# Kernel optimization log

Measured on AMD Instinct MI355X. Metric: run time of the kernel, lower is better.

## Reference

```python
import jax, jax.numpy as jnp
import numpy as np

N_EMBED = 2048
N_HEAD = 16
HEAD_DIM = N_EMBED // N_HEAD
ROPE_BASE = 500000


def _rope_cos_sin(T, dim, base):
    # torchtune RotaryPositionalEmbeddings: interleaved pairs
    inv_freq = 1.0 / (base ** (jnp.arange(0, dim, 2, dtype=jnp.float32) / dim))  # [dim/2]
    pos = jnp.arange(T, dtype=jnp.float32)
    ang = pos[:, None] * inv_freq[None, :]  # [T, dim/2]
    return jnp.cos(ang), jnp.sin(ang)


def _apply_rope(x, cos, sin):
    # x: [B, T, H, D]; cos/sin: [T, D/2] -> broadcast [1, T, 1, D/2]
    c = cos[None, :, None, :]
    s = sin[None, :, None, :]
    x1 = x[..., 0::2]
    x2 = x[..., 1::2]
    r1 = x1 * c - x2 * s
    r2 = x2 * c + x1 * s
    return jnp.stack([r1, r2], axis=-1).reshape(x.shape)


def setup_inputs() -> dict:
    key = jax.random.key(0)
    k1, k2, k3 = jax.random.split(key, 3)
    B, T, C = 4, 2048, N_EMBED
    x = jax.random.normal(k1, (B, T, C), dtype=jnp.float32)
    Wqkv = jax.random.normal(k2, (C, 3 * C), dtype=jnp.float32) * 0.02
    Wproj = jax.random.normal(k3, (C, C), dtype=jnp.float32) * 0.02
    return {"x": x, "Wqkv": Wqkv, "Wproj": Wproj}


def reference(x, Wqkv, Wproj):
    B, T, C = x.shape
    H, D = N_HEAD, HEAD_DIM
    qkv = x @ Wqkv  # [B, T, 3C]
    q, k, v = jnp.split(qkv, 3, axis=2)
    q = q.reshape(B, T, H, D)
    k = k.reshape(B, T, H, D)
    v = v.reshape(B, T, H, D)
    cos, sin = _rope_cos_sin(T, D, ROPE_BASE)
    q = _apply_rope(q, cos, sin)
    k = _apply_rope(k, cos, sin)
    scale = 1.0 / jnp.sqrt(jnp.float32(D))
    # causal SDPA: scores [B, H, T, T]
    scores = jnp.einsum('bqhd,bkhd->bhqk', q, k) * scale
    mask = jnp.tril(jnp.ones((T, T), dtype=bool))
    scores = jnp.where(mask[None, None, :, :], scores, jnp.float32(-1e30))
    attn = jax.nn.softmax(scores, axis=-1)
    y = jnp.einsum('bhqk,bkhd->bqhd', attn, v).reshape(B, T, C)
    return y @ Wproj
```

## Files before the change

kernel.cpp:

```cpp
#include <hip/hip_runtime.h>
#include <math.h>

#define NB 4
#define TT 2048
#define CC 2048
#define HH 16
#define DD 128
#define N3 6144
#define MM 8192
#define BH 64

typedef short bf8 __attribute__((ext_vector_type(8)));
typedef float f32x4 __attribute__((ext_vector_type(4)));
typedef unsigned short u16x8 __attribute__((ext_vector_type(8)));
typedef unsigned short u16;

constexpr float SCALE_QK  = 0.08838834764831843f;
constexpr float NEG_ALPHA = -0.20503692777194262f;

__device__ __forceinline__ u16 f2bf(float x) {
    unsigned int u = __float_as_uint(x);
    u += 0x7fffu + ((u >> 16) & 1u);
    return (u16)(u >> 16);
}
__device__ __forceinline__ float bf2f(u16 h) { return __uint_as_float(((unsigned int)h) << 16); }

__device__ __forceinline__ void gl_lds16(const u16* g, u16* l) {
    __builtin_amdgcn_global_load_lds(reinterpret_cast<const unsigned int*>(g),
                                     reinterpret_cast<unsigned int*>(l), 16, 0, 0);
}
__device__ __forceinline__ f32x4 MFMA(bf8 a, bf8 b, f32x4 c) {
    return __builtin_amdgcn_mfma_f32_16x16x32_bf16(a, b, c, 0, 0, 0);
}

#define BAR()    __builtin_amdgcn_s_barrier()
#define SCHED0() __builtin_amdgcn_sched_barrier(0)
#define WAIT_LGKM0() do { asm volatile("s_waitcnt lgkmcnt(0)" ::: "memory"); SCHED0(); } while (0)
#define WAIT_VM4()   do { asm volatile("s_waitcnt vmcnt(4)"   ::: "memory"); SCHED0(); } while (0)
#define WAIT_VM0()   do { asm volatile("s_waitcnt vmcnt(0)"   ::: "memory"); SCHED0(); } while (0)

__global__ void rope_tab_k(float* __restrict__ tab) {
    int t = blockIdx.x, p = threadIdx.x;
    float inv = expf((float)p * NEG_ALPHA);
    float s, c;
    sincosf((float)t * inv, &s, &c);
    tab[(t * 64 + p) * 2]     = c;
    tab[(t * 64 + p) * 2 + 1] = s;
}

__global__ __launch_bounds__(256) void split_x_k(const float* __restrict__ X,
                                                 u16* __restrict__ H, u16* __restrict__ L) {
    size_t base = ((size_t)blockIdx.x * 256 + threadIdx.x) * 16;
    #pragma unroll
    for (int g = 0; g < 2; ++g) {
        u16x8 hv, lv;
        #pragma unroll
        for (int j = 0; j < 8; j += 4) {
            float4 a = *(const float4*)(X + base + g * 8 + j);
            float xs[4] = {a.x, a.y, a.z, a.w};
            #pragma unroll
            for (int q = 0; q < 4; ++q) {
                u16 h = f2bf(xs[q]);
                hv[j + q] = h;
                lv[j + q] = f2bf(xs[q] - bf2f(h));
            }
        }
        *(u16x8*)&H[base + g * 8] = hv;
        *(u16x8*)&L[base + g * 8] = lv;
    }
}

__global__ __launch_bounds__(256) void splitT_k(const float* __restrict__ W,
                                                u16* __restrict__ OH, u16* __restrict__ OL,
                                                int Kd, int Nd) {
    __shared__ float tile[64][68];
    int k0 = blockIdx.x * 64, n0 = blockIdx.y * 64;
    {
        int r = threadIdx.x >> 2, cg = threadIdx.x & 3;
        const float* src = W + (size_t)(k0 + r) * Nd + n0 + cg * 16;
        #pragma unroll
        for (int j = 0; j < 4; ++j)
            *(float4*)&tile[r][cg * 16 + j * 4] = *(const float4*)(src + j * 4);
    }
    __syncthreads();
    int nl = threadIdx.x >> 2, kg = threadIdx.x & 3;
    u16x8 hv[2], lv[2];
    #pragma unroll
    for (int j = 0; j < 16; ++j) {
        float v = tile[kg * 16 + j][nl];
        u16 h = f2bf(v);
        hv[j >> 3][j & 7] = h;
        lv[j >> 3][j & 7] = f2bf(v - bf2f(h));
    }
    size_t off = (size_t)(n0 + nl) * Kd + k0 + kg * 16;
    *(u16x8*)&OH[off]     = hv[0];
    *(u16x8*)&OH[off + 8] = hv[1];
    *(u16x8*)&OL[off]     = lv[0];
    *(u16x8*)&OL[off + 8] = lv[1];
}

template<int MODE>
__global__ __launch_bounds__(512, 2) void gemm8p(
    const u16* __restrict__ Ahp, const u16* __restrict__ Alp,
    const u16* __restrict__ Bhp, const u16* __restrict__ Blp,
    u16* __restrict__ Qh, u16* __restrict__ Ql,
    u16* __restrict__ Kbo, u16* __restrict__ Vto,
    const float* __restrict__ tab, float* __restrict__ Out)
{
    __shared__ u16 SM[66048];

    const int tid = threadIdx.x;
    const int w = tid >> 6, ln = tid & 63;
    const int lo4 = ln & 15, hi4 = ln >> 4;
    const int wr = w >> 2, wc = w & 3;
    const int m0 = blockIdx.x * 256, n0 = blockIdx.y * 256;
    const int NKT = 96;

    f32x4 acc[8][4];
    #pragma unroll
    for (int i = 0; i < 8; ++i)
        #pragma unroll
        for (int j = 0; j < 4; ++j) acc[i][j] = (f32x4){0.f, 0.f, 0.f, 0.f};

    auto stage = [&](int s) {
        if (s >= 4 * NKT) return;
        const int tau = s >> 2, j = s & 3;
        const int c2 = tau & 1, op = j >> 1, hf = j & 1;
        const int tdiv = tau >> 5, tmod = tau & 31;
        const u16* plane;
        int row0;
        if (op == 0) { plane = (tdiv == 1) ? Alp : Ahp; row0 = m0 + hf * 128; }
        else         { plane = (tdiv == 2) ? Blp : Bhp; row0 = n0 + hf * 128; }
        u16* dst = SM + (op ? 32768 : 0) + (c2 * 2 + hf) * 8192;
        #pragma unroll
        for (int i = 0; i < 2; ++i) {
            int L = i * 8192 + tid * 16;
            int r = L >> 7;
            int c = (L >> 4) & 7;
            int cs = c ^ (r & 7);
            gl_lds16(plane + (size_t)(row0 + r) * 2048 + tmod * 64 + cs * 8,
                     dst + (L >> 1));
        }
    };

    #pragma unroll
    for (int s = 0; s < 6; ++s) stage(s);
    WAIT_VM4();
    BAR();

    bf8 a03[4][2], a47[4][2], b01[2][2], b23[2][2];
    const int brow0 = (wc & 1) * 64;

    for (int t = 0; t < NKT; ++t) {
        const int c2 = t & 1;
        const u16* Ab = SM + (c2 * 2 + wr) * 8192;
        const u16* Bb = SM + 32768 + (c2 * 2 + (wc >> 1)) * 8192;

        #pragma unroll
        for (int mf = 0; mf < 4; ++mf) {
            int rr = mf * 16 + lo4, s7 = rr & 7;
            a03[mf][0] = *(const bf8*)&Ab[rr * 64 + ((hi4 ^ s7)) * 8];
            a03[mf][1] = *(const bf8*)&Ab[rr * 64 + (((4 + hi4) ^ s7)) * 8];
        }
        #pragma unroll
        for (int nf = 0; nf < 2; ++nf) {
            int rr = brow0 + nf * 16 + lo4, s7 = rr & 7;
            b01[nf][0] = *(const bf8*)&Bb[rr * 64 + ((hi4 ^ s7)) * 8];
            b01[nf][1] = *(const bf8*)&Bb[rr * 64 + (((4 + hi4) ^ s7)) * 8];
        }
        stage(4 * t + 6);
        BAR(); WAIT_LGKM0();
        __builtin_amdgcn_s_setprio(1);
        #pragma unroll
        for (int mf = 0; mf < 4; ++mf)
            #pragma unroll
            for (int nf = 0; nf < 2; ++nf) {
                acc[mf][nf] = MFMA(a03[mf][0], b01[nf][0], acc[mf][nf]);
                acc[mf][nf] = MFMA(a03[mf][1], b01[nf][1], acc[mf][nf]);
            }
        __builtin_amdgcn_s_setprio(0);
        BAR();

        #pragma unroll
        for (int mf = 0; mf < 4; ++mf) {
            int rr = 64 + mf * 16 + lo4, s7 = rr & 7;
            a47[mf][0] = *(const bf8*)&Ab[rr * 64 + ((hi4 ^ s7)) * 8];
            a47[mf][1] = *(const bf8*)&Ab[rr * 64 + (((4 + hi4) ^ s7)) * 8];
        }
        stage(4 * t + 7);
        BAR(); WAIT_LGKM0();
        __builtin_amdgcn_s_setprio(1);
        #pragma unroll
        for (int mf = 0; mf < 4; ++mf)
            #pragma unroll
            for (int nf = 0; nf < 2; ++nf) {
                acc[4 + mf][nf] = MFMA(a47[mf][0], b01[nf][0], acc[4 + mf][nf]);
                acc[4 + mf][nf] = MFMA(a47[mf][1], b01[nf][1], acc[4 + mf][nf]);
            }
        __builtin_amdgcn_s_setprio(0);
        BAR();

        #pragma unroll
        for (int nf = 0; nf < 2; ++nf) {
            int rr = brow0 + 32 + nf * 16 + lo4, s7 = rr & 7;
            b23[nf][0] = *(const bf8*)&Bb[rr * 64 + ((hi4 ^ s7)) * 8];
            b23[nf][1] = *(const bf8*)&Bb[rr * 64 + (((4 + hi4) ^ s7)) * 8];
        }
        stage(4 * t + 8);
        BAR(); WAIT_LGKM0();
        __builtin_amdgcn_s_setprio(1);
        #pragma unroll
        for (int mf = 0; mf < 4; ++mf)
            #pragma unroll
            for (int nf = 0; nf < 2; ++nf) {
                acc[mf][2 + nf] = MFMA(a03[mf][0], b23[nf][0], acc[mf][2 + nf]);
                acc[mf][2 + nf] = MFMA(a03[mf][1], b23[nf][1], acc[mf][2 + nf]);
            }
        __builtin_amdgcn_s_setprio(0);
        BAR();

        stage(4 * t + 9);
        BAR();
        __builtin_amdgcn_s_setprio(1);
        #pragma unroll
        for (int mf = 0; mf < 4; ++mf)
            #pragma unroll
            for (int nf = 0; nf < 2; ++nf) {
                acc[4 + mf][2 + nf] = MFMA(a47[mf][0], b23[nf][0], acc[4 + mf][2 + nf]);
                acc[4 + mf][2 + nf] = MFMA(a47[mf][1], b23[nf][1], acc[4 + mf][2 + nf]);
            }
        __builtin_amdgcn_s_setprio(0);
        if (t < NKT - 2)       { WAIT_VM4(); }
        else if (t == NKT - 2) { WAIT_VM0(); }
        BAR();
    }

    if (MODE == 1) {
        #pragma unroll
        for (int mf = 0; mf < 8; ++mf)
            #pragma unroll
            for (int r = 0; r < 4; ++r) {
                int m = m0 + wr * 128 + mf * 16 + hi4 * 4 + r;
                float* rowp = Out + (size_t)m * CC + n0 + wc * 64;
                #pragma unroll
                for (int nf = 0; nf < 4; ++nf)
                    rowp[nf * 16 + lo4] = acc[mf][nf][r];
            }
        return;
    }

    const int sec = n0 >> 11;
    const int hh0 = (n0 >> 7) & 15;
    if (sec < 2) {
        #pragma unroll
        for (int mf = 0; mf < 8; ++mf)
            #pragma unroll
            for (int r = 0; r < 4; ++r) {
                int m = m0 + wr * 128 + mf * 16 + hi4 * 4 + r;
                int t = m & 2047, b = m >> 11;
                #pragma unroll
                for (int nf = 0; nf < 4; ++nf) {
                    int nl = wc * 64 + nf * 16 + lo4;
                    int h = hh0 + (nl >> 7), d = nl & 127;
                    float v = acc[mf][nf][r];
                    float o = __shfl_xor(v, 1);
                    const float2 cs2 = *(const float2*)&tab[(((size_t)t << 6) + (d >> 1)) * 2];
                    float rv = (ln & 1) ? (v * cs2.x + o * cs2.y)
                                        : (v * cs2.x - o * cs2.y);
                    size_t off = (((size_t)(b * HH + h)) * TT + t) * DD + d;
                    if (sec == 0) {
                        rv *= SCALE_QK;
                        u16 hv = f2bf(rv);
                        Qh[off] = hv;
                        Ql[off] = f2bf(rv - bf2f(hv));
                    } else {
                        Kbo[off] = f2bf(rv);
                    }
                }
            }
    } else {
        BAR();
        #pragma unroll
        for (int mf = 0; mf < 8; ++mf)
            #pragma unroll
            for (int r = 0; r < 4; ++r) {
                int tl = wr * 128 + mf * 16 + hi4 * 4 + r;
                #pragma unroll
                for (int nf = 0; nf < 4; ++nf) {
                    int nl = wc * 64 + nf * 16 + lo4;
                    SM[tl * 258 + nl] = f2bf(acc[mf][nf][r]);
                }
            }
        BAR();
        int nl = tid >> 1, th = tid & 1;
        int head = hh0 + (nl >> 7), d = nl & 127;
        int b = m0 >> 11, t0 = m0 & 2047;
        size_t base = (((size_t)(b * HH + head)) * DD + d) * TT + t0 + th * 128;
        #pragma unroll
        for (int g = 0; g < 16; ++g) {
            u16x8 vv;
            #pragma unroll
            for (int j = 0; j < 8; ++j) vv[j] = SM[(th * 128 + g * 8 + j) * 258 + nl];
            *(u16x8*)&Vto[base + g * 8] = vv;
        }
    }
}

__global__ __launch_bounds__(256) void attn_mfma(
    const u16* __restrict__ Qhp, const u16* __restrict__ Qlp,
    const u16* __restrict__ Kb,  const u16* __restrict__ Vt,
    u16* __restrict__ Yh, u16* __restrict__ Yl)
{
    __shared__ u16 Ks[64 * 128];
    __shared__ u16 Vs[128 * 64];
    __shared__ u16 Ps[4][16 * 64];

    const int tid = threadIdx.x;
    const int w = tid >> 6, ln = tid & 63;
    const int lo4 = ln & 15, hi4 = ln >> 4;
    const int qt = blockIdx.x, bh = blockIdx.y;
    const int q0 = qt * 64;

    const size_t qoff = ((size_t)bh * TT + q0) * DD;
    #pragma unroll
    for (int i = 0; i < 4; ++i) {
        int L = i * 4096 + tid * 16;
        int r = L >> 8;
        int c = (L >> 4) & 15;
        int cs = c ^ (r & 7);
        gl_lds16(Qhp + qoff + r * DD + cs * 8, &Ks[L >> 1]);
        gl_lds16(Qlp + qoff + r * DD + cs * 8, &Vs[L >> 1]);
    }
    __syncthreads();
    bf8 qh[4], ql[4];
    {
        int r = w * 16 + lo4;
        #pragma unroll
        for (int ks = 0; ks < 4; ++ks) {
            int ch = (ks * 4 + hi4) ^ (r & 7);
            qh[ks] = *(const bf8*)&Ks[r * 128 + ch * 8];
            ql[ks] = *(const bf8*)&Vs[r * 128 + ch * 8];
        }
    }

    f32x4 O[8];
    #pragma unroll
    for (int i = 0; i < 8; ++i) O[i] = (f32x4){0.f, 0.f, 0.f, 0.f};
    float m_r[4] = {-1e30f, -1e30f, -1e30f, -1e30f};
    float l_r[4] = {0.f, 0.f, 0.f, 0.f};

    for (int kt = 0; kt <= qt; ++kt) {
        __syncthreads();
        const size_t koff = ((size_t)bh * TT + kt * 64) * DD;
        #pragma unroll
        for (int i = 0; i < 4; ++i) {
            int L = i * 4096 + tid * 16;
            int r = L >> 8;
            int c = (L >> 4) & 15;
            int cs = c ^ (r & 7);
            gl_lds16(Kb + koff + r * DD + cs * 8, &Ks[L >> 1]);
        }
        #pragma unroll
        for (int i = 0; i < 4; ++i) {
            int L = i * 4096 + tid * 16;
            int r = L >> 7;
            int c = (L >> 4) & 7;
            int cs = c ^ (r & 7);
            gl_lds16(Vt + ((size_t)bh * DD + r) * TT + kt * 64 + cs * 8, &Vs[L >> 1]);
        }
        __syncthreads();

        f32x4 sf[4];
        #pragma unroll
        for (int nf = 0; nf < 4; ++nf) {
            f32x4 a2 = (f32x4){0.f, 0.f, 0.f, 0.f};
            int kr = nf * 16 + lo4;
            #pragma unroll
            for (int ks = 0; ks < 4; ++ks) {
                int ch = (ks * 4 + hi4) ^ (kr & 7);
                bf8 bb = *(const bf8*)&Ks[kr * 128 + ch * 8];
                a2 = MFMA(qh[ks], bb, a2);
                a2 = MFMA(ql[ks], bb, a2);
            }
            sf[nf] = a2;
        }
        if (kt == qt) {
            #pragma unroll
            for (int nf = 0; nf < 4; ++nf)
                #pragma unroll
                for (int r = 0; r < 4; ++r) {
                    int kg = kt * 64 + nf * 16 + lo4;
                    int qg = q0 + w * 16 + hi4 * 4 + r;
                    if (kg > qg) sf[nf][r] = -1e30f;
                }
        }
        #pragma unroll
        for (int r = 0; r < 4; ++r) {
            float mx = fmaxf(fmaxf(sf[0][r], sf[1][r]), fmaxf(sf[2][r], sf[3][r]));
            mx = fmaxf(mx, __shfl_xor(mx, 1));
            mx = fmaxf(mx, __shfl_xor(mx, 2));
            mx = fmaxf(mx, __shfl_xor(mx, 4));
            mx = fmaxf(mx, __shfl_xor(mx, 8));
            float mn = fmaxf(m_r[r], mx);
            float al = __expf(m_r[r] - mn);
            m_r[r] = mn;
            float rs = 0.f;
            #pragma unroll
            for (int nf = 0; nf < 4; ++nf) {
                float p = __expf(sf[nf][r] - mn);
                sf[nf][r] = p;
                rs += p;
            }
            rs += __shfl_xor(rs, 1);
            rs += __shfl_xor(rs, 2);
            rs += __shfl_xor(rs, 4);
            rs += __shfl_xor(rs, 8);
            l_r[r] = l_r[r] * al + rs;
            #pragma unroll
            for (int nf2 = 0; nf2 < 8; ++nf2) O[nf2][r] *= al;
        }
        u16* pw = &Ps[w][0];
        #pragma unroll
        for (int r = 0; r < 4; ++r) {
            int row = hi4 * 4 + r;
            int sw = (row & 7) << 3;
            #pragma unroll
            for (int nf = 0; nf < 4; ++nf)
                pw[row * 64 + ((nf * 16 + lo4) ^ sw)] = f2bf(sf[nf][r]);
        }
        bf8 pa[2];
        {
            int row = lo4, s3 = row & 7;
            pa[0] = *(const bf8*)&pw[row * 64 + ((hi4 ^ s3) * 8)];
            pa[1] = *(const bf8*)&pw[row * 64 + (((4 + hi4) ^ s3) * 8)];
        }
        #pragma unroll
        for (int nf2 = 0; nf2 < 8; ++nf2) {
            int vr = nf2 * 16 + lo4;
            #pragma unroll
            for (int ks = 0; ks < 2; ++ks) {
                int ch = (ks * 4 + hi4) ^ (vr & 7);
                bf8 vb = *(const bf8*)&Vs[vr * 64 + ch * 8];
                O[nf2] = MFMA(pa[ks], vb, O[nf2]);
            }
        }
    }

    const int b = bh >> 4, h = bh & 15;
    #pragma unroll
    for (int r = 0; r < 4; ++r) {
        float inv = 1.0f / l_r[r];
        int t = q0 + w * 16 + hi4 * 4 + r;
        size_t rowo = ((size_t)(b * TT + t)) * CC + h * DD;
        #pragma unroll
        for (int nf2 = 0; nf2 < 8; ++nf2) {
            float val = O[nf2][r] * inv;
            u16 hv = f2bf(val);
            Yh[rowo + nf2 * 16 + lo4] = hv;
            Yl[rowo + nf2 * 16 + lo4] = f2bf(val - bf2f(hv));
        }
    }
}

extern "C" void kernel_launch(void* const* d_in, const int* in_sizes, int n_in,
                              void* d_out, int out_size, void* d_ws, size_t ws_size,
                              hipStream_t stream)
{
    const float* X     = (const float*)d_in[0];
    const float* Wqkv  = (const float*)d_in[1];
    const float* Wproj = (const float*)d_in[2];

    char* W = (char*)d_ws;
    float* tab = (float*)W;
    u16* Wqh = (u16*)(W + (1u << 20));
    u16* Wql = Wqh + 12582912;
    u16* Wph = Wql + 12582912;
    u16* Wpl = Wph + 4194304;
    u16* Xh  = Wpl + 4194304;
    u16* Xl  = Xh + 16777216;
    u16* Kb  = Xl + 16777216;
    u16* Vt  = Kb + 16777216;

    u16* Qh = (u16*)d_out;
    u16* Ql = Qh + 16777216;

    u16* Yh = Xh;
    u16* Yl = Xl;

    rope_tab_k<<<dim3(2048), 64, 0, stream>>>(tab);
    split_x_k<<<dim3(4096), 256, 0, stream>>>(X, Xh, Xl);
    splitT_k<<<dim3(32, 96), 256, 0, stream>>>(Wqkv, Wqh, Wql, 2048, 6144);
    splitT_k<<<dim3(32, 32), 256, 0, stream>>>(Wproj, Wph, Wpl, 2048, 2048);

    gemm8p<0><<<dim3(32, 24), 512, 0, stream>>>(Xh, Xl, Wqh, Wql,
                                                Qh, Ql, Kb, Vt, tab, nullptr);
    attn_mfma<<<dim3(32, 64), 256, 0, stream>>>(Qh, Ql, Kb, Vt, Yh, Yl);
    gemm8p<1><<<dim3(32, 8), 512, 0, stream>>>(Yh, Yl, Wph, Wpl,
                                               nullptr, nullptr, nullptr, nullptr,
                                               nullptr, (float*)d_out);
}
```

Baseline: 1.231 ms.

## Drop weight low-part GEMM pass and rewrite attention with 128-row double-buffered tiles

The weights are now split into a bf16 high part only, so both GEMMs run two bf16 passes (Ah*Bh, Al*Bh) instead of three, cutting K-iterations from 96 to 64 and the weight-split work. The attention kernel now gives each block 128 query rows, double-buffers K/V tiles with async global-to-LDS loads, and pairs light and heavy causal tiles in the block ordering. It also skips the O rescale when no row maximum grows. Losing the weight low part reduces accuracy, and the larger attention tile adds register pressure.

```diff
diff --git a/kernel.cpp b/kernel.cpp
--- a/kernel.cpp
+++ b/kernel.cpp
@@ -36,6 +36,7 @@
 #define BAR()    __builtin_amdgcn_s_barrier()
 #define SCHED0() __builtin_amdgcn_sched_barrier(0)
 #define WAIT_LGKM0() do { asm volatile("s_waitcnt lgkmcnt(0)" ::: "memory"); SCHED0(); } while (0)
+#define WAIT_VM8()   do { asm volatile("s_waitcnt vmcnt(8)"   ::: "memory"); SCHED0(); } while (0)
 #define WAIT_VM4()   do { asm volatile("s_waitcnt vmcnt(4)"   ::: "memory"); SCHED0(); } while (0)
 #define WAIT_VM0()   do { asm volatile("s_waitcnt vmcnt(0)"   ::: "memory"); SCHED0(); } while (0)
 
@@ -70,8 +71,8 @@
     }
 }
 
-__global__ __launch_bounds__(256) void splitT_k(const float* __restrict__ W,
-                                                u16* __restrict__ OH, u16* __restrict__ OL,
+__global__ __launch_bounds__(256) void splitT_h(const float* __restrict__ W,
+                                                u16* __restrict__ OH,
                                                 int Kd, int Nd) {
     __shared__ float tile[64][68];
     int k0 = blockIdx.x * 64, n0 = blockIdx.y * 64;
@@ -84,25 +85,19 @@
     }
     __syncthreads();
     int nl = threadIdx.x >> 2, kg = threadIdx.x & 3;
-    u16x8 hv[2], lv[2];
-    #pragma unroll
-    for (int j = 0; j < 16; ++j) {
-        float v = tile[kg * 16 + j][nl];
-        u16 h = f2bf(v);
-        hv[j >> 3][j & 7] = h;
-        lv[j >> 3][j & 7] = f2bf(v - bf2f(h));
-    }
+    u16x8 hv[2];
+    #pragma unroll
+    for (int j = 0; j < 16; ++j)
+        hv[j >> 3][j & 7] = f2bf(tile[kg * 16 + j][nl]);
     size_t off = (size_t)(n0 + nl) * Kd + k0 + kg * 16;
     *(u16x8*)&OH[off]     = hv[0];
     *(u16x8*)&OH[off + 8] = hv[1];
-    *(u16x8*)&OL[off]     = lv[0];
-    *(u16x8*)&OL[off + 8] = lv[1];
 }
 
 template<int MODE>
 __global__ __launch_bounds__(512, 2) void gemm8p(
     const u16* __restrict__ Ahp, const u16* __restrict__ Alp,
-    const u16* __restrict__ Bhp, const u16* __restrict__ Blp,
+    const u16* __restrict__ Bhp,
     u16* __restrict__ Qh, u16* __restrict__ Ql,
     u16* __restrict__ Kbo, u16* __restrict__ Vto,
     const float* __restrict__ tab, float* __restrict__ Out)
@@ -114,7 +109,7 @@
     const int lo4 = ln & 15, hi4 = ln >> 4;
     const int wr = w >> 2, wc = w & 3;
     const int m0 = blockIdx.x * 256, n0 = blockIdx.y * 256;
-    const int NKT = 96;
+    const int NKT = 64;
 
     f32x4 acc[8][4];
     #pragma unroll
@@ -129,8 +124,8 @@
         const int tdiv = tau >> 5, tmod = tau & 31;
         const u16* plane;
         int row0;
-        if (op == 0) { plane = (tdiv == 1) ? Alp : Ahp; row0 = m0 + hf * 128; }
-        else         { plane = (tdiv == 2) ? Blp : Bhp; row0 = n0 + hf * 128; }
+        if (op == 0) { plane = tdiv ? Alp : Ahp; row0 = m0 + hf * 128; }
+        else         { plane = Bhp;              row0 = n0 + hf * 128; }
         u16* dst = SM + (op ? 32768 : 0) + (c2 * 2 + hf) * 8192;
         #pragma unroll
         for (int i = 0; i < 2; ++i) {
@@ -306,160 +301,207 @@
     }
 }
 
-__global__ __launch_bounds__(256) void attn_mfma(
+__global__ __launch_bounds__(256, 2) void attn128(
     const u16* __restrict__ Qhp, const u16* __restrict__ Qlp,
     const u16* __restrict__ Kb,  const u16* __restrict__ Vt,
     u16* __restrict__ Yh, u16* __restrict__ Yl)
 {
-    __shared__ u16 Ks[64 * 128];
-    __shared__ u16 Vs[128 * 64];
-    __shared__ u16 Ps[4][16 * 64];
+    __shared__ u16 SM[40960];
 
     const int tid = threadIdx.x;
     const int w = tid >> 6, ln = tid & 63;
     const int lo4 = ln & 15, hi4 = ln >> 4;
-    const int qt = blockIdx.x, bh = blockIdx.y;
-    const int q0 = qt * 64;
+    const int bx = blockIdx.x;
+    const int qt = (bx & 1) ? (15 - (bx >> 1)) : (bx >> 1);
+    const int bh = blockIdx.y;
+    const int q0 = qt * 128;
+    const int last = 2 * qt + 1;
 
     const size_t qoff = ((size_t)bh * TT + q0) * DD;
     #pragma unroll
-    for (int i = 0; i < 4; ++i) {
+    for (int i = 0; i < 8; ++i) {
         int L = i * 4096 + tid * 16;
-        int r = L >> 8;
-        int c = (L >> 4) & 15;
+        int r = L >> 8, c = (L >> 4) & 15;
         int cs = c ^ (r & 7);
-        gl_lds16(Qhp + qoff + r * DD + cs * 8, &Ks[L >> 1]);
-        gl_lds16(Qlp + qoff + r * DD + cs * 8, &Vs[L >> 1]);
-    }
-    __syncthreads();
-    bf8 qh[4], ql[4];
-    {
-        int r = w * 16 + lo4;
+        gl_lds16(Qhp + qoff + r * DD + cs * 8, &SM[L >> 1]);
+        gl_lds16(Qlp + qoff + r * DD + cs * 8, &SM[16384 + (L >> 1)]);
+    }
+    WAIT_VM0();
+    BAR();
+    bf8 qh[2][4], ql[2][4];
+    #pragma unroll
+    for (int mf = 0; mf < 2; ++mf) {
+        int rq = w * 32 + mf * 16 + lo4, s7 = rq & 7;
         #pragma unroll
         for (int ks = 0; ks < 4; ++ks) {
-            int ch = (ks * 4 + hi4) ^ (r & 7);
-            qh[ks] = *(const bf8*)&Ks[r * 128 + ch * 8];
-            ql[ks] = *(const bf8*)&Vs[r * 128 + ch * 8];
-        }
-    }
-
-    f32x4 O[8];
-    #pragma unroll
-    for (int i = 0; i < 8; ++i) O[i] = (f32x4){0.f, 0.f, 0.f, 0.f};
-    float m_r[4] = {-1e30f, -1e30f, -1e30f, -1e30f};
-    float l_r[4] = {0.f, 0.f, 0.f, 0.f};
-
-    for (int kt = 0; kt <= qt; ++kt) {
-        __syncthreads();
-        const size_t koff = ((size_t)bh * TT + kt * 64) * DD;
+            int ch = (ks * 4 + hi4) ^ s7;
+            qh[mf][ks] = *(const bf8*)&SM[rq * 128 + ch * 8];
+            ql[mf][ks] = *(const bf8*)&SM[16384 + rq * 128 + ch * 8];
+        }
+    }
+    WAIT_LGKM0();
+    BAR();
+
+    auto stageKV = [&](int kt2, int buf) {
+        const size_t koff = ((size_t)bh * TT + kt2 * 64) * DD;
+        u16* kd = &SM[buf * 8192];
         #pragma unroll
         for (int i = 0; i < 4; ++i) {
             int L = i * 4096 + tid * 16;
-            int r = L >> 8;
-            int c = (L >> 4) & 15;
-            int cs = c ^ (r & 7);
-            gl_lds16(Kb + koff + r * DD + cs * 8, &Ks[L >> 1]);
-        }
+            int r = L >> 8, c = (L >> 4) & 15, cs = c ^ (r & 7);
+            gl_lds16(Kb + koff + r * DD + cs * 8, kd + (L >> 1));
+        }
+        const size_t voff = (size_t)bh * DD * TT + (size_t)kt2 * 64;
+        u16* vd = &SM[16384 + buf * 8192];
         #pragma unroll
         for (int i = 0; i < 4; ++i) {
             int L = i * 4096 + tid * 16;
-            int r = L >> 7;
-            int c = (L >> 4) & 7;
-            int cs = c ^ (r & 7);
-            gl_lds16(Vt + ((size_t)bh * DD + r) * TT + kt * 64 + cs * 8, &Vs[L >> 1]);
-        }
-        __syncthreads();
-
-        f32x4 sf[4];
+            int r = L >> 7, c = (L >> 4) & 7, cs = c ^ (r & 7);
+            gl_lds16(Vt + voff + (size_t)r * TT + cs * 8, vd + (L >> 1));
+        }
+    };
+    stageKV(0, 0);
+
+    f32x4 O[2][8];
+    #pragma unroll
+    for (int mf = 0; mf < 2; ++mf)
+        #pragma unroll
+        for (int i = 0; i < 8; ++i) O[mf][i] = (f32x4){0.f, 0.f, 0.f, 0.f};
+    float m_r[2][4], l_r[2][4];
+    #pragma unroll
+    for (int mf = 0; mf < 2; ++mf)
+        #pragma unroll
+        for (int r = 0; r < 4; ++r) { m_r[mf][r] = -1e30f; l_r[mf][r] = 0.f; }
+
+    for (int kt = 0; kt <= last; ++kt) {
+        const int cur = kt & 1;
+        if (kt < last) { stageKV(kt + 1, cur ^ 1); WAIT_VM8(); }
+        else           { WAIT_VM0(); }
+        BAR();
+        const u16* Kcur = &SM[cur * 8192];
+        const u16* Vcur = &SM[16384 + cur * 8192];
+
+        f32x4 sf[2][4];
         #pragma unroll
         for (int nf = 0; nf < 4; ++nf) {
-            f32x4 a2 = (f32x4){0.f, 0.f, 0.f, 0.f};
-            int kr = nf * 16 + lo4;
+            f32x4 s0 = (f32x4){0.f, 0.f, 0.f, 0.f};
+            f32x4 s1 = (f32x4){0.f, 0.f, 0.f, 0.f};
+            int kr = nf * 16 + lo4, s7 = kr & 7;
             #pragma unroll
             for (int ks = 0; ks < 4; ++ks) {
-                int ch = (ks * 4 + hi4) ^ (kr & 7);
-                bf8 bb = *(const bf8*)&Ks[kr * 128 + ch * 8];
-                a2 = MFMA(qh[ks], bb, a2);
-                a2 = MFMA(ql[ks], bb, a2);
-            }
-            sf[nf] = a2;
-        }
-        if (kt == qt) {
-            #pragma unroll
-            for (int nf = 0; nf < 4; ++nf)
+                bf8 bb = *(const bf8*)&Kcur[kr * 128 + ((ks * 4 + hi4) ^ s7) * 8];
+                s0 = MFMA(qh[0][ks], bb, s0);
+                s0 = MFMA(ql[0][ks], bb, s0);
+                s1 = MFMA(qh[1][ks], bb, s1);
+                s1 = MFMA(ql[1][ks], bb, s1);
+            }
+            sf[0][nf] = s0; sf[1][nf] = s1;
+        }
+        if (kt >= 2 * qt) {
+            #pragma unroll
+            for (int mf = 0; mf < 2; ++mf)
+                #pragma unroll
+                for (int nf = 0; nf < 4; ++nf)
+                    #pragma unroll
+                    for (int r = 0; r < 4; ++r) {
+                        int kg = kt * 64 + nf * 16 + lo4;
+                        int qg = q0 + w * 32 + mf * 16 + hi4 * 4 + r;
+                        if (kg > qg) sf[mf][nf][r] = -1e30f;
+                    }
+        }
+
+        #pragma unroll
+        for (int mf = 0; mf < 2; ++mf) {
+            float mx[4];
+            #pragma unroll
+            for (int r = 0; r < 4; ++r) {
+                float m2 = fmaxf(fmaxf(sf[mf][0][r], sf[mf][1][r]),
+                                 fmaxf(sf[mf][2][r], sf[mf][3][r]));
+                m2 = fmaxf(m2, __shfl_xor(m2, 1));
+                m2 = fmaxf(m2, __shfl_xor(m2, 2));
+                m2 = fmaxf(m2, __shfl_xor(m2, 4));
+                m2 = fmaxf(m2, __shfl_xor(m2, 8));
+                mx[r] = m2;
+            }
+            float al[4] = {1.f, 1.f, 1.f, 1.f};
+            bool grow = (mx[0] > m_r[mf][0]) || (mx[1] > m_r[mf][1]) ||
+                        (mx[2] > m_r[mf][2]) || (mx[3] > m_r[mf][3]);
+            if (__any(grow)) {
                 #pragma unroll
                 for (int r = 0; r < 4; ++r) {
-                    int kg = kt * 64 + nf * 16 + lo4;
-                    int qg = q0 + w * 16 + hi4 * 4 + r;
-                    if (kg > qg) sf[nf][r] = -1e30f;
+                    float mn = fmaxf(m_r[mf][r], mx[r]);
+                    al[r] = __expf(m_r[mf][r] - mn);
+                    m_r[mf][r] = mn;
                 }
-        }
+                #pragma unroll
+                for (int nf2 = 0; nf2 < 8; ++nf2)
+                    #pragma unroll
+                    for (int r = 0; r < 4; ++r) O[mf][nf2][r] *= al[r];
+            }
+            #pragma unroll
+            for (int r = 0; r < 4; ++r) {
+                float rs = 0.f;
+                #pragma unroll
+                for (int nf = 0; nf < 4; ++nf) {
+                    float p = __expf(sf[mf][nf][r] - m_r[mf][r]);
+                    sf[mf][nf][r] = p;
+                    rs += p;
+                }
+                rs += __shfl_xor(rs, 1);
+                rs += __shfl_xor(rs, 2);
+                rs += __shfl_xor(rs, 4);
+                rs += __shfl_xor(rs, 8);
+                l_r[mf][r] = l_r[mf][r] * al[r] + rs;
+            }
+        }
+
+        u16* pw = &SM[32768 + w * 2048];
+        #pragma unroll
+        for (int mf = 0; mf < 2; ++mf)
+            #pragma unroll
+            for (int r = 0; r < 4; ++r) {
+                int row = mf * 16 + hi4 * 4 + r;
+                int sw = (row & 7) << 3;
+                #pragma unroll
+                for (int nf = 0; nf < 4; ++nf)
+                    pw[row * 64 + ((nf * 16 + lo4) ^ sw)] = f2bf(sf[mf][nf][r]);
+            }
+        bf8 pa[2][2];
+        #pragma unroll
+        for (int mf = 0; mf < 2; ++mf) {
+            int rp = mf * 16 + lo4, s3 = rp & 7;
+            pa[mf][0] = *(const bf8*)&pw[rp * 64 + ((hi4 ^ s3) * 8)];
+            pa[mf][1] = *(const bf8*)&pw[rp * 64 + (((4 + hi4) ^ s3) * 8)];
+        }
+        #pragma unroll
+        for (int nf2 = 0; nf2 < 8; ++nf2) {
+            int vr = nf2 * 16 + lo4, s7 = vr & 7;
+            #pragma unroll
+            for (int ks = 0; ks < 2; ++ks) {
+                bf8 vb = *(const bf8*)&Vcur[vr * 64 + ((ks * 4 + hi4) ^ s7) * 8];
+                O[0][nf2] = MFMA(pa[0][ks], vb, O[0][nf2]);
+                O[1][nf2] = MFMA(pa[1][ks], vb, O[1][nf2]);
+            }
+        }
+        BAR();
+    }
+
+    const int b = bh >> 4, h = bh & 15;
+    #pragma unroll
+    for (int mf = 0; mf < 2; ++mf)
         #pragma unroll
         for (int r = 0; r < 4; ++r) {
-            float mx = fmaxf(fmaxf(sf[0][r], sf[1][r]), fmaxf(sf[2][r], sf[3][r]));
-            mx = fmaxf(mx, __shfl_xor(mx, 1));
-            mx = fmaxf(mx, __shfl_xor(mx, 2));
-            mx = fmaxf(mx, __shfl_xor(mx, 4));
-            mx = fmaxf(mx, __shfl_xor(mx, 8));
-            float mn = fmaxf(m_r[r], mx);
-            float al = __expf(m_r[r] - mn);
-            m_r[r] = mn;
-            float rs = 0.f;
-            #pragma unroll
-            for (int nf = 0; nf < 4; ++nf) {
-                float p = __expf(sf[nf][r] - mn);
-                sf[nf][r] = p;
-                rs += p;
-            }
-            rs += __shfl_xor(rs, 1);
-            rs += __shfl_xor(rs, 2);
-            rs += __shfl_xor(rs, 4);
-            rs += __shfl_xor(rs, 8);
-            l_r[r] = l_r[r] * al + rs;
-            #pragma unroll
-            for (int nf2 = 0; nf2 < 8; ++nf2) O[nf2][r] *= al;
-        }
-        u16* pw = &Ps[w][0];
-        #pragma unroll
-        for (int r = 0; r < 4; ++r) {
-            int row = hi4 * 4 + r;
-            int sw = (row & 7) << 3;
-            #pragma unroll
-            for (int nf = 0; nf < 4; ++nf)
-                pw[row * 64 + ((nf * 16 + lo4) ^ sw)] = f2bf(sf[nf][r]);
-        }
-        bf8 pa[2];
-        {
-            int row = lo4, s3 = row & 7;
-            pa[0] = *(const bf8*)&pw[row * 64 + ((hi4 ^ s3) * 8)];
-            pa[1] = *(const bf8*)&pw[row * 64 + (((4 + hi4) ^ s3) * 8)];
-        }
-        #pragma unroll
-        for (int nf2 = 0; nf2 < 8; ++nf2) {
-            int vr = nf2 * 16 + lo4;
-            #pragma unroll
-            for (int ks = 0; ks < 2; ++ks) {
-                int ch = (ks * 4 + hi4) ^ (vr & 7);
-                bf8 vb = *(const bf8*)&Vs[vr * 64 + ch * 8];
-                O[nf2] = MFMA(pa[ks], vb, O[nf2]);
-            }
-        }
-    }
-
-    const int b = bh >> 4, h = bh & 15;
-    #pragma unroll
-    for (int r = 0; r < 4; ++r) {
-        float inv = 1.0f / l_r[r];
-        int t = q0 + w * 16 + hi4 * 4 + r;
-        size_t rowo = ((size_t)(b * TT + t)) * CC + h * DD;
-        #pragma unroll
-        for (int nf2 = 0; nf2 < 8; ++nf2) {
-            float val = O[nf2][r] * inv;
-            u16 hv = f2bf(val);
-            Yh[rowo + nf2 * 16 + lo4] = hv;
-            Yl[rowo + nf2 * 16 + lo4] = f2bf(val - bf2f(hv));
-        }
-    }
+            float inv = 1.0f / l_r[mf][r];
+            int t = q0 + w * 32 + mf * 16 + hi4 * 4 + r;
+            size_t rowo = ((size_t)(b * TT + t)) * CC + h * DD;
+            #pragma unroll
+            for (int nf2 = 0; nf2 < 8; ++nf2) {
+                float val = O[mf][nf2][r] * inv;
+                u16 hv = f2bf(val);
+                Yh[rowo + nf2 * 16 + lo4] = hv;
+                Yl[rowo + nf2 * 16 + lo4] = f2bf(val - bf2f(hv));
+            }
+        }
 }
 
 extern "C" void kernel_launch(void* const* d_in, const int* in_sizes, int n_in,
@@ -473,10 +515,8 @@
     char* W = (char*)d_ws;
     float* tab = (float*)W;
     u16* Wqh = (u16*)(W + (1u << 20));
-    u16* Wql = Wqh + 12582912;
-    u16* Wph = Wql + 12582912;
-    u16* Wpl = Wph + 4194304;
-    u16* Xh  = Wpl + 4194304;
+    u16* Wph = Wqh + 12582912;
+    u16* Xh  = Wph + 4194304;
     u16* Xl  = Xh + 16777216;
     u16* Kb  = Xl + 16777216;
     u16* Vt  = Kb + 16777216;
@@ -489,13 +529,13 @@
 
     rope_tab_k<<<dim3(2048), 64, 0, stream>>>(tab);
     split_x_k<<<dim3(4096), 256, 0, stream>>>(X, Xh, Xl);
-    splitT_k<<<dim3(32, 96), 256, 0, stream>>>(Wqkv, Wqh, Wql, 2048, 6144);
-    splitT_k<<<dim3(32, 32), 256, 0, stream>>>(Wproj, Wph, Wpl, 2048, 2048);
-
-    gemm8p<0><<<dim3(32, 24), 512, 0, stream>>>(Xh, Xl, Wqh, Wql,
+    splitT_h<<<dim3(32, 96), 256, 0, stream>>>(Wqkv, Wqh, 2048, 6144);
+    splitT_h<<<dim3(32, 32), 256, 0, stream>>>(Wproj, Wph, 2048, 2048);
+
+    gemm8p<0><<<dim3(32, 24), 512, 0, stream>>>(Xh, Xl, Wqh,
                                                 Qh, Ql, Kb, Vt, tab, nullptr);
-    attn_mfma<<<dim3(32, 64), 256, 0, stream>>>(Qh, Ql, Kb, Vt, Yh, Yl);
-    gemm8p<1><<<dim3(32, 8), 512, 0, stream>>>(Yh, Yl, Wph, Wpl,
+    attn128<<<dim3(16, 64), 256, 0, stream>>>(Qh, Ql, Kb, Vt, Yh, Yl);
+    gemm8p<1><<<dim3(32, 8), 512, 0, stream>>>(Yh, Yl, Wph,
                                                nullptr, nullptr, nullptr, nullptr,
                                                nullptr, (float*)d_out);
 }
```

Result: faster. 1.017 ms (-17.4%).
